# Optimization experiments

Hardware: AMD Instinct MI355X
Metric: run time of the kernel (lower is better)

Reference implementation:

```python
import jax, jax.numpy as jnp
import numpy as np

B, T, C, H = 2, 2048, 1024, 16
DH = C // H  # 64


def setup_inputs() -> dict:
    key = jax.random.key(0)
    ks = jax.random.split(key, 8)
    scale = 1.0 / np.sqrt(C)
    x = jax.random.normal(ks[0], (B, T, C), dtype=jnp.float32)
    mask = jax.random.randint(ks[1], (B, T), 0, 2, dtype=jnp.int32)
    Wq = jax.random.normal(ks[2], (C, C), dtype=jnp.float32) * scale
    bq = jnp.zeros((C,), dtype=jnp.float32)
    Wk = jax.random.normal(ks[3], (C, C), dtype=jnp.float32) * scale
    bk = jnp.zeros((C,), dtype=jnp.float32)
    Wv = jax.random.normal(ks[4], (C, C), dtype=jnp.float32) * scale
    bv = jnp.zeros((C,), dtype=jnp.float32)
    return {"x": x, "Wq": Wq, "bq": bq, "Wk": Wk, "bk": bk, "Wv": Wv, "bv": bv, "mask": mask}


def reference(x, Wq, bq, Wk, bk, Wv, bv, mask):
    # q/k/v projections: [B,T,C] -> [B,H,T,DH]
    def proj(W, b):
        return (x @ W + b).reshape(B, T, H, DH).transpose(0, 2, 1, 3)

    q = proj(Wq, bq)
    k = proj(Wk, bk)
    v = proj(Wv, bv)

    att = jnp.einsum("bhqd,bhkd->bhqk", q, k) * (1.0 / np.sqrt(DH))

    # outer-product padding mask: square_mask[b,q,k] = mask[b,q]*mask[b,k]
    m = mask.astype(jnp.float32)
    square_mask = m[:, :, None] * m[:, None, :]           # [B,T,T]
    sm = (square_mask != 0)[:, None, :, :]                 # [B,1,T,T]
    att = jnp.where(sm, att, -jnp.inf)

    # rows that are fully masked (query token padded) -> softmax gives NaN
    # in torch; torch then zeros the NaNs. Replicate with a safe softmax.
    row_valid = (mask != 0)[:, None, :, None]              # [B,1,T,1]
    att_safe = jnp.where(row_valid, att, 0.0)
    att = jax.nn.softmax(att_safe, axis=-1)
    att = jnp.where(row_valid, att, 0.0)
    # attn_pdrop = 0.0 -> dropout is identity

    y = jnp.einsum("bhqk,bhkd->bhqd", att, v)              # [B,H,T,DH]
    y = y.transpose(0, 2, 1, 3).reshape(B, T, C)
    return y
```

## Files before the change

### kernel.cpp

```cpp
#include <hip/hip_runtime.h>

#define B_ 2
#define T_ 2048
#define C_ 1024
#define H_ 16
#define DH_ 64

typedef __attribute__((ext_vector_type(8))) _Float16 half8;
typedef __attribute__((ext_vector_type(2))) __fp16 fp16x2;
typedef __attribute__((ext_vector_type(4))) float f32x4;

__device__ __forceinline__ unsigned short f2h(float f) {
    union { _Float16 h; unsigned short u; } cv; cv.h = (_Float16)f; return cv.u;
}
__device__ __forceinline__ unsigned pk2(float a, float b) {
    union { fp16x2 h; unsigned u; } cv;
    cv.h = __builtin_amdgcn_cvt_pkrtz(a, b);
    return cv.u;
}

__device__ __forceinline__ void gll16(const void* g, void* l) {
    __builtin_amdgcn_global_load_lds(
        (const __attribute__((address_space(1))) void*)g,
        (__attribute__((address_space(3))) void*)l, 16, 0, 0);
}

__global__ __launch_bounds__(256) void prep_x_kernel(
    const float* __restrict__ x, unsigned short* __restrict__ xf,
    const int* __restrict__ mask, unsigned short* __restrict__ mb)
{
    const size_t idx8 = ((size_t)blockIdx.x * 256 + threadIdx.x) * 8;
    float4 v0 = *(const float4*)(x + idx8);
    float4 v1 = *(const float4*)(x + idx8 + 4);
    float f[8] = {v0.x, v0.y, v0.z, v0.w, v1.x, v1.y, v1.z, v1.w};
    unsigned short h[8];
#pragma unroll
    for (int i = 0; i < 8; i++) h[i] = f2h(f[i]);
    *(uint4*)(xf + idx8) = *(const uint4*)h;

    if (blockIdx.x == 0) {
#pragma unroll
        for (int j = 0; j < 16; j++) {
            int i = threadIdx.x * 16 + j;
            mb[i] = (mask[i] != 0) ? (unsigned short)0x3C00 : (unsigned short)0;
        }
    }
}

__global__ __launch_bounds__(256) void prep_w_kernel(
    const float* __restrict__ Wq, const float* __restrict__ Wk,
    const float* __restrict__ Wv, unsigned short* __restrict__ wt)
{
    __shared__ float tile[32][33];
    const int z = blockIdx.z;
    const float* __restrict__ W = (z == 0) ? Wq : (z == 1) ? Wk : Wv;
    unsigned short* __restrict__ wtz = wt + (size_t)z * C_ * C_;
    const int n0 = blockIdx.x * 32;
    const int k0 = blockIdx.y * 32;
    const int tx = threadIdx.x;
    const int ty = threadIdx.y;
#pragma unroll
    for (int j = 0; j < 4; j++)
        tile[ty + j * 8][tx] = W[(size_t)(k0 + ty + j * 8) * C_ + n0 + tx];
    __syncthreads();
#pragma unroll
    for (int j = 0; j < 4; j++)
        wtz[(size_t)(n0 + ty + j * 8) * C_ + k0 + tx] = f2h(tile[tx][ty + j * 8]);
}

__global__ __launch_bounds__(256) void qkv_mfma_kernel(
    const unsigned short* __restrict__ xf, const unsigned short* __restrict__ wt,
    const float* __restrict__ bq, const float* __restrict__ bk,
    const float* __restrict__ bv, const int* __restrict__ maskp,
    unsigned short* __restrict__ qb, unsigned short* __restrict__ kb,
    unsigned short* __restrict__ vt)
{
    __shared__ unsigned short sX[128 * 64];
    __shared__ unsigned short sW[128 * 64];

    const int z = blockIdx.z;
    const float* __restrict__ bias = (z == 0) ? bq : (z == 1) ? bk : bv;
    const unsigned short* __restrict__ wtz = wt + (size_t)z * C_ * C_;

    const int tok0 = blockIdx.x * 128;
    const int col0 = blockIdx.y * 128;
    const int wv    = threadIdx.x >> 6;
    const int lane  = threadIdx.x & 63;
    const int l15   = lane & 15;
    const int quad  = lane >> 4;
    const int l7    = l15 & 7;
    const int wm    = wv >> 1;
    const int wn    = wv & 1;
    const int lrow8 = lane >> 3;
    const int gch   = (lane & 7) ^ lrow8;

    f32x4 acc[4][4];
#pragma unroll
    for (int i = 0; i < 4; i++)
#pragma unroll
        for (int j = 0; j < 4; j++) acc[i][j] = (f32x4){0.f, 0.f, 0.f, 0.f};

    int aoff[4][2], boff[4][2];
#pragma unroll
    for (int i = 0; i < 4; i++)
#pragma unroll
        for (int s = 0; s < 2; s++) {
            aoff[i][s] = (wm * 64 + i * 16 + l15) * 64 + (((s * 4 + quad) ^ l7) * 8);
            boff[i][s] = (wn * 64 + i * 16 + l15) * 64 + (((s * 4 + quad) ^ l7) * 8);
        }

    const unsigned short* Abuf = (z < 2) ? sX : sW;
    const unsigned short* Bbuf = (z < 2) ? sW : sX;

    for (int k0 = 0; k0 < C_; k0 += 64) {
        __syncthreads();
#pragma unroll
        for (int s = 0; s < 8; ++s) {
            int g    = (s << 2) + wv;
            int tsel = g >> 4;
            int r0   = (g & 15) << 3;
            const unsigned short* src = tsel ? wtz : xf;
            unsigned short*       dst = tsel ? sW  : sX;
            int rowg = tsel ? col0 : tok0;
            gll16(src + (size_t)(rowg + r0 + lrow8) * C_ + k0 + gch * 8,
                  dst + r0 * 64);
        }
        __syncthreads();

        half8 af[4][2], bf_[4][2];
#pragma unroll
        for (int i = 0; i < 4; i++)
#pragma unroll
            for (int s = 0; s < 2; s++) {
                af[i][s]  = *(const half8*)&Abuf[aoff[i][s]];
                bf_[i][s] = *(const half8*)&Bbuf[boff[i][s]];
            }
#pragma unroll
        for (int s = 0; s < 2; s++)
#pragma unroll
            for (int j = 0; j < 4; j++)
#pragma unroll
                for (int i = 0; i < 4; i++)
                    acc[i][j] = __builtin_amdgcn_mfma_f32_16x16x32_f16(
                        af[i][s], bf_[j][s], acc[i][j], 0, 0, 0);
    }

    if (z < 2) {
        unsigned short* outp = (z == 0) ? qb : kb;
#pragma unroll
        for (int j = 0; j < 4; j++) {
            int col = col0 + wn * 64 + j * 16 + l15;
            int h = col >> 6, d = col & 63;
            float bs = bias[col];
#pragma unroll
            for (int i = 0; i < 4; i++) {
#pragma unroll
                for (int r = 0; r < 4; r++) {
                    int tok = tok0 + wm * 64 + i * 16 + quad * 4 + r;
                    int bidx = tok >> 11, t = tok & (T_ - 1);
                    outp[((size_t)(bidx * H_ + h) * T_ + t) * DH_ + d] =
                        f2h(acc[i][j][r] + bs);
                }
            }
        }
    } else {
        float mv4[4]; int bidx4[4], t4[4];
#pragma unroll
        for (int j = 0; j < 4; j++) {
            int tok = tok0 + wn * 64 + j * 16 + l15;
            bidx4[j] = tok >> 11; t4[j] = tok & (T_ - 1);
            mv4[j] = (maskp[bidx4[j] * T_ + t4[j]] != 0) ? 1.f : 0.f;
        }
#pragma unroll
        for (int i = 0; i < 4; i++) {
#pragma unroll
            for (int r = 0; r < 4; r++) {
                int col = col0 + wm * 64 + i * 16 + quad * 4 + r;
                int h = col >> 6, d = col & 63;
                float bs = bias[col];
#pragma unroll
                for (int j = 0; j < 4; j++) {
                    vt[((size_t)(bidx4[j] * H_ + h) * DH_ + d) * T_ + t4[j]] =
                        f2h((acc[i][j][r] + bs) * mv4[j]);
                }
            }
        }
    }
}

__global__ __launch_bounds__(256) void attn_mfma_kernel(
    const unsigned short* __restrict__ qb,
    const unsigned short* __restrict__ kb,
    const unsigned short* __restrict__ vt,
    const int* __restrict__ mask,
    const unsigned short* __restrict__ mb,
    float* __restrict__ out)
{
    __shared__ unsigned short Ks[2][64 * 64];
    __shared__ unsigned short Vs[2][64 * 64];
    __shared__ unsigned short Ps[4][16 * 64];

    const int bh   = blockIdx.x;
    const int b    = bh >> 4;
    const int h    = bh & 15;
    const int wv   = threadIdx.x >> 6;
    const int lane = threadIdx.x & 63;
    const int l15  = lane & 15;
    const int quad = lane >> 4;
    const int l7   = l15 & 7;
    const int q0w  = blockIdx.y * 128 + wv * 32;

    const unsigned short* kbh = kb + (size_t)bh * T_ * DH_;
    const unsigned short* vbh = vt + (size_t)bh * DH_ * T_;
    const unsigned short* mbb = mb + b * T_;
    const int* __restrict__ mrow = mask + b * T_;

    half8 qf[2][2];
#pragma unroll
    for (int qt = 0; qt < 2; ++qt)
#pragma unroll
        for (int c = 0; c < 2; ++c)
            qf[qt][c] = *(const half8*)(qb + ((size_t)bh * T_ + q0w + qt * 16 + l15) * DH_
                                        + c * 32 + quad * 8);

    f32x4 o[2][4];
#pragma unroll
    for (int qt = 0; qt < 2; ++qt)
#pragma unroll
        for (int n = 0; n < 4; ++n) o[qt][n] = (f32x4){0.f, 0.f, 0.f, 0.f};
    f32x4 lacc[2];
    lacc[0] = (f32x4){0.f, 0.f, 0.f, 0.f};
    lacc[1] = (f32x4){0.f, 0.f, 0.f, 0.f};

    const int lrow = lane >> 3;
    const int gch  = (lane & 7) ^ lrow;

#pragma unroll
    for (int s = 0; s < 4; ++s) {
        int j  = (wv << 2) + s;
        int rb = j & 7;
        if (j < 8) gll16(kbh + (size_t)(rb * 8 + lrow) * DH_ + gch * 8, &Ks[0][rb * 512]);
        else       gll16(vbh + (size_t)(rb * 8 + lrow) * T_  + gch * 8, &Vs[0][rb * 512]);
    }

    for (int kt = 0; kt < 32; ++kt) {
        const int cur   = kt & 1;
        const int kbase = kt * 64;
        __syncthreads();

        if (kt < 31) {
            const int nb = kbase + 64;
#pragma unroll
            for (int s = 0; s < 4; ++s) {
                int j  = (wv << 2) + s;
                int rb = j & 7;
                if (j < 8) gll16(kbh + (size_t)(nb + rb * 8 + lrow) * DH_ + gch * 8,
                                 &Ks[cur ^ 1][rb * 512]);
                else       gll16(vbh + (size_t)(rb * 8 + lrow) * T_ + nb + gch * 8,
                                 &Vs[cur ^ 1][rb * 512]);
            }
        }

        const unsigned short* Kc = &Ks[cur][0];
        const unsigned short* Vc = &Vs[cur][0];

        half8 kf[4][2], vf[4][2];
#pragma unroll
        for (int ktile = 0; ktile < 4; ++ktile)
#pragma unroll
            for (int c = 0; c < 2; ++c) {
                kf[ktile][c] = *(const half8*)(Kc + (ktile * 16 + l15) * 64
                                               + (((c * 4 + quad) ^ l7) * 8));
                vf[ktile][c] = *(const half8*)(Vc + (ktile * 16 + l15) * 64
                                               + (((c * 4 + quad) ^ l7) * 8));
            }

        half8 bmf[2];
#pragma unroll
        for (int kc = 0; kc < 2; ++kc) {
            half8 mv = *(const half8*)(mbb + kbase + kc * 32 + quad * 8);
            bmf[kc] = (l15 == 0) ? mv : (half8)0;
        }

#pragma unroll
        for (int qt = 0; qt < 2; ++qt) {
            unsigned short* Pq = &Ps[wv][0];

#pragma unroll
            for (int ktile = 0; ktile < 4; ++ktile) {
                f32x4 st = (f32x4){0.f, 0.f, 0.f, 0.f};
                st = __builtin_amdgcn_mfma_f32_16x16x32_f16(kf[ktile][0], qf[qt][0], st, 0, 0, 0);
                st = __builtin_amdgcn_mfma_f32_16x16x32_f16(kf[ktile][1], qf[qt][1], st, 0, 0, 0);
                float p0 = __builtin_amdgcn_exp2f(fminf(st[0] * 0.18033688011112042f, 14.f));
                float p1 = __builtin_amdgcn_exp2f(fminf(st[1] * 0.18033688011112042f, 14.f));
                float p2 = __builtin_amdgcn_exp2f(fminf(st[2] * 0.18033688011112042f, 14.f));
                float p3 = __builtin_amdgcn_exp2f(fminf(st[3] * 0.18033688011112042f, 14.f));
                uint2 pk;
                pk.x = pk2(p0, p1);
                pk.y = pk2(p2, p3);
                *(uint2*)(Pq + l15 * 64 + (((ktile * 2 + (quad >> 1)) ^ l7) * 8)
                          + (quad & 1) * 4) = pk;
            }

            half8 pf[2];
#pragma unroll
            for (int kc = 0; kc < 2; ++kc)
                pf[kc] = *(const half8*)(Pq + l15 * 64 + (((kc * 4 + quad) ^ l7) * 8));

            lacc[qt] = __builtin_amdgcn_mfma_f32_16x16x32_f16(pf[0], bmf[0], lacc[qt], 0, 0, 0);
            lacc[qt] = __builtin_amdgcn_mfma_f32_16x16x32_f16(pf[1], bmf[1], lacc[qt], 0, 0, 0);

#pragma unroll
            for (int n = 0; n < 4; ++n) {
#pragma unroll
                for (int kc = 0; kc < 2; ++kc)
                    o[qt][n] = __builtin_amdgcn_mfma_f32_16x16x32_f16(
                        pf[kc], vf[n][kc], o[qt][n], 0, 0, 0);
            }
        }
    }

#pragma unroll
    for (int qt = 0; qt < 2; ++qt) {
#pragma unroll
        for (int r = 0; r < 4; ++r) {
            float lv = __shfl(lacc[qt][r], quad << 4, 64);
            int q = q0w + qt * 16 + quad * 4 + r;
            float iv = (mrow[q] != 0 && lv > 0.f) ? (1.0f / lv) : 0.f;
            float* orow = out + ((size_t)(b * T_ + q)) * C_ + h * DH_;
#pragma unroll
            for (int n = 0; n < 4; ++n)
                orow[n * 16 + l15] = o[qt][n][r] * iv;
        }
    }
}

extern "C" void kernel_launch(void* const* d_in, const int* in_sizes, int n_in,
                              void* d_out, int out_size, void* d_ws, size_t ws_size,
                              hipStream_t stream)
{
    (void)in_sizes; (void)n_in; (void)out_size; (void)ws_size;
    const float* x  = (const float*)d_in[0];
    const float* Wq = (const float*)d_in[1];
    const float* bq = (const float*)d_in[2];
    const float* Wk = (const float*)d_in[3];
    const float* bk = (const float*)d_in[4];
    const float* Wv = (const float*)d_in[5];
    const float* bv = (const float*)d_in[6];
    const int* mask = (const int*)d_in[7];
    float* out = (float*)d_out;

    const size_t NX = (size_t)B_ * T_ * C_;
    unsigned short* xf = (unsigned short*)d_ws;
    unsigned short* wt = xf + NX;
    unsigned short* qb = wt + (size_t)3 * C_ * C_;
    unsigned short* kb = qb + NX;
    unsigned short* vt = kb + NX;
    unsigned short* mb = vt + NX;

    prep_x_kernel<<<2048, 256, 0, stream>>>(x, xf, mask, mb);
    prep_w_kernel<<<dim3(32, 32, 3), dim3(32, 8), 0, stream>>>(Wq, Wk, Wv, wt);
    qkv_mfma_kernel<<<dim3(32, 8, 3), 256, 0, stream>>>(
        xf, wt, bq, bk, bv, mask, qb, kb, vt);
    attn_mfma_kernel<<<dim3(32, 16), 256, 0, stream>>>(qb, kb, vt, mask, mb, out);
}
```

Measured before the change: 177.7 us.

## Split attention key range across two blocks and add a combine kernel

Adds a second grid dimension so each attention block handles half of the key sequence (1024 keys), doubling the number of blocks to raise GPU occupancy. Each half writes unnormalized partial outputs and per-row softmax denominators; a new combine kernel sums the two partials, applies the mask, and normalizes. This works because the kernel accumulates exp sums without a running max, so partials add linearly. The cost is an extra kernel launch plus writing and re-reading a full fp32 partial output. That partial buffer reuses the workspace left by the x/W conversion buffers and may extend past them.

```diff
diff --git a/kernel.cpp b/kernel.cpp
--- a/kernel.cpp
+++ b/kernel.cpp
@@ -192,9 +192,10 @@
     const unsigned short* __restrict__ qb,
     const unsigned short* __restrict__ kb,
     const unsigned short* __restrict__ vt,
-    const int* __restrict__ mask,
     const unsigned short* __restrict__ mb,
-    float* __restrict__ out)
+    float* __restrict__ po0,
+    float* __restrict__ po1,
+    float* __restrict__ lw)
 {
     __shared__ unsigned short Ks[2][64 * 64];
     __shared__ unsigned short Vs[2][64 * 64];
@@ -203,6 +204,8 @@
     const int bh   = blockIdx.x;
     const int b    = bh >> 4;
     const int h    = bh & 15;
+    const int kh   = blockIdx.z;
+    const int kh0  = kh << 10;
     const int wv   = threadIdx.x >> 6;
     const int lane = threadIdx.x & 63;
     const int l15  = lane & 15;
@@ -210,10 +213,12 @@
     const int l7   = l15 & 7;
     const int q0w  = blockIdx.y * 128 + wv * 32;
 
+    float* __restrict__ po = kh ? po1 : po0;
+    float* __restrict__ lwk = lw + (size_t)kh * B_ * T_ * H_;
+
     const unsigned short* kbh = kb + (size_t)bh * T_ * DH_;
     const unsigned short* vbh = vt + (size_t)bh * DH_ * T_;
     const unsigned short* mbb = mb + b * T_;
-    const int* __restrict__ mrow = mask + b * T_;
 
     half8 qf[2][2];
 #pragma unroll
@@ -239,16 +244,16 @@
     for (int s = 0; s < 4; ++s) {
         int j  = (wv << 2) + s;
         int rb = j & 7;
-        if (j < 8) gll16(kbh + (size_t)(rb * 8 + lrow) * DH_ + gch * 8, &Ks[0][rb * 512]);
-        else       gll16(vbh + (size_t)(rb * 8 + lrow) * T_  + gch * 8, &Vs[0][rb * 512]);
-    }
-
-    for (int kt = 0; kt < 32; ++kt) {
+        if (j < 8) gll16(kbh + (size_t)(kh0 + rb * 8 + lrow) * DH_ + gch * 8, &Ks[0][rb * 512]);
+        else       gll16(vbh + (size_t)(rb * 8 + lrow) * T_ + kh0 + gch * 8, &Vs[0][rb * 512]);
+    }
+
+    for (int kt = 0; kt < 16; ++kt) {
         const int cur   = kt & 1;
-        const int kbase = kt * 64;
+        const int kbase = kh0 + kt * 64;
         __syncthreads();
 
-        if (kt < 31) {
+        if (kt < 15) {
             const int nb = kbase + 64;
 #pragma unroll
             for (int s = 0; s < 4; ++s) {
@@ -324,15 +329,40 @@
     for (int qt = 0; qt < 2; ++qt) {
 #pragma unroll
         for (int r = 0; r < 4; ++r) {
-            float lv = __shfl(lacc[qt][r], quad << 4, 64);
             int q = q0w + qt * 16 + quad * 4 + r;
-            float iv = (mrow[q] != 0 && lv > 0.f) ? (1.0f / lv) : 0.f;
-            float* orow = out + ((size_t)(b * T_ + q)) * C_ + h * DH_;
+            float* orow = po + ((size_t)(b * T_ + q)) * C_ + h * DH_;
 #pragma unroll
             for (int n = 0; n < 4; ++n)
-                orow[n * 16 + l15] = o[qt][n][r] * iv;
-        }
-    }
+                orow[n * 16 + l15] = o[qt][n][r];
+            if (l15 == 0)
+                lwk[((size_t)(b * T_ + q)) * H_ + h] = lacc[qt][r];
+        }
+    }
+}
+
+__global__ __launch_bounds__(256) void combine_kernel(
+    const float* __restrict__ po1, const float* __restrict__ lw,
+    const int* __restrict__ mask, float* __restrict__ out)
+{
+    const size_t e = ((size_t)blockIdx.x * 256 + threadIdx.x) * 8;
+    const int h = (int)((e >> 6) & 15);
+    const int q = (int)((e >> 10) & (T_ - 1));
+    const int b = (int)(e >> 21);
+
+    float4 a0 = *(const float4*)(out + e);
+    float4 a1 = *(const float4*)(out + e + 4);
+    float4 c0 = *(const float4*)(po1 + e);
+    float4 c1 = *(const float4*)(po1 + e + 4);
+    size_t li = ((size_t)(b * T_ + q)) * H_ + h;
+    float l = lw[li] + lw[(size_t)B_ * T_ * H_ + li];
+    float iv = (mask[b * T_ + q] != 0 && l > 0.f) ? (1.0f / l) : 0.f;
+
+    float4 r0 = {(a0.x + c0.x) * iv, (a0.y + c0.y) * iv,
+                 (a0.z + c0.z) * iv, (a0.w + c0.w) * iv};
+    float4 r1 = {(a1.x + c1.x) * iv, (a1.y + c1.y) * iv,
+                 (a1.z + c1.z) * iv, (a1.w + c1.w) * iv};
+    *(float4*)(out + e)     = r0;
+    *(float4*)(out + e + 4) = r1;
 }
 
 extern "C" void kernel_launch(void* const* d_in, const int* in_sizes, int n_in,
@@ -351,16 +381,20 @@
     float* out = (float*)d_out;
 
     const size_t NX = (size_t)B_ * T_ * C_;
-    unsigned short* xf = (unsigned short*)d_ws;
-    unsigned short* wt = xf + NX;
-    unsigned short* qb = wt + (size_t)3 * C_ * C_;
+    unsigned short* qb = (unsigned short*)d_ws;
     unsigned short* kb = qb + NX;
     unsigned short* vt = kb + NX;
     unsigned short* mb = vt + NX;
+    unsigned short* xf = mb + (size_t)B_ * T_;
+    unsigned short* wt = xf + NX;
+    float* po1 = (float*)xf;
+    float* lw  = po1 + NX;
 
     prep_x_kernel<<<2048, 256, 0, stream>>>(x, xf, mask, mb);
     prep_w_kernel<<<dim3(32, 32, 3), dim3(32, 8), 0, stream>>>(Wq, Wk, Wv, wt);
     qkv_mfma_kernel<<<dim3(32, 8, 3), 256, 0, stream>>>(
         xf, wt, bq, bk, bv, mask, qb, kb, vt);
-    attn_mfma_kernel<<<dim3(32, 16), 256, 0, stream>>>(qb, kb, vt, mask, mb, out);
-}
+    attn_mfma_kernel<<<dim3(32, 16, 2), 256, 0, stream>>>(
+        qb, kb, vt, mb, out, po1, lw);
+    combine_kernel<<<2048, 256, 0, stream>>>(po1, lw, mask, out);
+}
```

Measured after the change: 189.6 us. 6.7% more time.

## Store K/V in MFMA fragment order and load directly to registers

Applied to the files above, without the earlier changes.

The QKV projection now writes K and V into a pre-swizzled fragment-major layout that matches the per-lane MFMA operand order. This lets the attention kernel read each fragment with contiguous 16-byte global loads instead of staging K/V tiles through double-buffered LDS with global_load_lds and a per-iteration barrier. The per-wave P buffer is also split per query tile, which avoids reuse hazards without sync. In exchange, every wave fetches K/V from global memory or L2 on its own with no sharing across the block, and there is no explicit prefetch to hide load latency.

```diff
diff --git a/kernel.cpp b/kernel.cpp
--- a/kernel.cpp
+++ b/kernel.cpp
@@ -23,6 +23,15 @@
     __builtin_amdgcn_global_load_lds(
         (const __attribute__((address_space(1))) void*)g,
         (__attribute__((address_space(3))) void*)l, 16, 0, 0);
+}
+
+__device__ __forceinline__ size_t kidx(int bh, int key, int d) {
+    return ((size_t)(bh * 128 + (key >> 4)) * 2 + (d >> 5)) * 512
+         + (size_t)((((d >> 3) & 3) * 16 + (key & 15)) * 8 + (d & 7));
+}
+__device__ __forceinline__ size_t vidx(int bh, int key, int d) {
+    return (((size_t)(bh * 32 + (key >> 6)) * 4 + (d >> 4)) * 2 + ((key >> 5) & 1)) * 512
+         + (size_t)((((key >> 3) & 3) * 16 + (d & 15)) * 8 + (key & 7));
 }
 
 __global__ __launch_bounds__(256) void prep_x_kernel(
@@ -72,8 +81,8 @@
     const unsigned short* __restrict__ xf, const unsigned short* __restrict__ wt,
     const float* __restrict__ bq, const float* __restrict__ bk,
     const float* __restrict__ bv, const int* __restrict__ maskp,
-    unsigned short* __restrict__ qb, unsigned short* __restrict__ kb,
-    unsigned short* __restrict__ vt)
+    unsigned short* __restrict__ qb, unsigned short* __restrict__ kfr,
+    unsigned short* __restrict__ vfr)
 {
     __shared__ unsigned short sX[128 * 64];
     __shared__ unsigned short sW[128 * 64];
@@ -145,8 +154,7 @@
                         af[i][s], bf_[j][s], acc[i][j], 0, 0, 0);
     }
 
-    if (z < 2) {
-        unsigned short* outp = (z == 0) ? qb : kb;
+    if (z == 0) {
 #pragma unroll
         for (int j = 0; j < 4; j++) {
             int col = col0 + wn * 64 + j * 16 + l15;
@@ -158,8 +166,24 @@
                 for (int r = 0; r < 4; r++) {
                     int tok = tok0 + wm * 64 + i * 16 + quad * 4 + r;
                     int bidx = tok >> 11, t = tok & (T_ - 1);
-                    outp[((size_t)(bidx * H_ + h) * T_ + t) * DH_ + d] =
+                    qb[((size_t)(bidx * H_ + h) * T_ + t) * DH_ + d] =
                         f2h(acc[i][j][r] + bs);
+                }
+            }
+        }
+    } else if (z == 1) {
+#pragma unroll
+        for (int j = 0; j < 4; j++) {
+            int col = col0 + wn * 64 + j * 16 + l15;
+            int h = col >> 6, d = col & 63;
+            float bs = bias[col];
+#pragma unroll
+            for (int i = 0; i < 4; i++) {
+#pragma unroll
+                for (int r = 0; r < 4; r++) {
+                    int tok = tok0 + wm * 64 + i * 16 + quad * 4 + r;
+                    int bidx = tok >> 11, t = tok & (T_ - 1);
+                    kfr[kidx(bidx * H_ + h, t, d)] = f2h(acc[i][j][r] + bs);
                 }
             }
         }
@@ -180,7 +204,7 @@
                 float bs = bias[col];
 #pragma unroll
                 for (int j = 0; j < 4; j++) {
-                    vt[((size_t)(bidx4[j] * H_ + h) * DH_ + d) * T_ + t4[j]] =
+                    vfr[vidx(bidx4[j] * H_ + h, t4[j], d)] =
                         f2h((acc[i][j][r] + bs) * mv4[j]);
                 }
             }
@@ -190,15 +214,13 @@
 
 __global__ __launch_bounds__(256) void attn_mfma_kernel(
     const unsigned short* __restrict__ qb,
-    const unsigned short* __restrict__ kb,
-    const unsigned short* __restrict__ vt,
+    const unsigned short* __restrict__ kfr,
+    const unsigned short* __restrict__ vfr,
     const int* __restrict__ mask,
     const unsigned short* __restrict__ mb,
     float* __restrict__ out)
 {
-    __shared__ unsigned short Ks[2][64 * 64];
-    __shared__ unsigned short Vs[2][64 * 64];
-    __shared__ unsigned short Ps[4][16 * 64];
+    __shared__ unsigned short Ps[4][2][16 * 64];
 
     const int bh   = blockIdx.x;
     const int b    = bh >> 4;
@@ -210,10 +232,11 @@
     const int l7   = l15 & 7;
     const int q0w  = blockIdx.y * 128 + wv * 32;
 
-    const unsigned short* kbh = kb + (size_t)bh * T_ * DH_;
-    const unsigned short* vbh = vt + (size_t)bh * DH_ * T_;
     const unsigned short* mbb = mb + b * T_;
     const int* __restrict__ mrow = mask + b * T_;
+
+    const unsigned short* kfp = kfr + (size_t)bh * 131072 + lane * 8;
+    const unsigned short* vfp = vfr + (size_t)bh * 131072 + lane * 8;
 
     half8 qf[2][2];
 #pragma unroll
@@ -232,48 +255,17 @@
     lacc[0] = (f32x4){0.f, 0.f, 0.f, 0.f};
     lacc[1] = (f32x4){0.f, 0.f, 0.f, 0.f};
 
-    const int lrow = lane >> 3;
-    const int gch  = (lane & 7) ^ lrow;
-
-#pragma unroll
-    for (int s = 0; s < 4; ++s) {
-        int j  = (wv << 2) + s;
-        int rb = j & 7;
-        if (j < 8) gll16(kbh + (size_t)(rb * 8 + lrow) * DH_ + gch * 8, &Ks[0][rb * 512]);
-        else       gll16(vbh + (size_t)(rb * 8 + lrow) * T_  + gch * 8, &Vs[0][rb * 512]);
-    }
-
     for (int kt = 0; kt < 32; ++kt) {
-        const int cur   = kt & 1;
         const int kbase = kt * 64;
-        __syncthreads();
-
-        if (kt < 31) {
-            const int nb = kbase + 64;
-#pragma unroll
-            for (int s = 0; s < 4; ++s) {
-                int j  = (wv << 2) + s;
-                int rb = j & 7;
-                if (j < 8) gll16(kbh + (size_t)(nb + rb * 8 + lrow) * DH_ + gch * 8,
-                                 &Ks[cur ^ 1][rb * 512]);
-                else       gll16(vbh + (size_t)(rb * 8 + lrow) * T_ + nb + gch * 8,
-                                 &Vs[cur ^ 1][rb * 512]);
-            }
-        }
-
-        const unsigned short* Kc = &Ks[cur][0];
-        const unsigned short* Vc = &Vs[cur][0];
 
         half8 kf[4][2], vf[4][2];
 #pragma unroll
-        for (int ktile = 0; ktile < 4; ++ktile)
-#pragma unroll
-            for (int c = 0; c < 2; ++c) {
-                kf[ktile][c] = *(const half8*)(Kc + (ktile * 16 + l15) * 64
-                                               + (((c * 4 + quad) ^ l7) * 8));
-                vf[ktile][c] = *(const half8*)(Vc + (ktile * 16 + l15) * 64
-                                               + (((c * 4 + quad) ^ l7) * 8));
-            }
+        for (int s = 0; s < 8; ++s)
+            kf[s >> 1][s & 1] = *(const half8*)(kfp + s * 512);
+#pragma unroll
+        for (int s = 0; s < 8; ++s)
+            vf[s >> 1][s & 1] = *(const half8*)(vfp + s * 512);
+        kfp += 4096; vfp += 4096;
 
         half8 bmf[2];
 #pragma unroll
@@ -284,7 +276,7 @@
 
 #pragma unroll
         for (int qt = 0; qt < 2; ++qt) {
-            unsigned short* Pq = &Ps[wv][0];
+            unsigned short* Pq = &Ps[wv][qt][0];
 
 #pragma unroll
             for (int ktile = 0; ktile < 4; ++ktile) {
@@ -351,16 +343,16 @@
     float* out = (float*)d_out;
 
     const size_t NX = (size_t)B_ * T_ * C_;
-    unsigned short* xf = (unsigned short*)d_ws;
-    unsigned short* wt = xf + NX;
-    unsigned short* qb = wt + (size_t)3 * C_ * C_;
-    unsigned short* kb = qb + NX;
-    unsigned short* vt = kb + NX;
-    unsigned short* mb = vt + NX;
+    unsigned short* xf  = (unsigned short*)d_ws;
+    unsigned short* wt  = xf + NX;
+    unsigned short* qb  = wt + (size_t)3 * C_ * C_;
+    unsigned short* kfr = qb + NX;
+    unsigned short* vfr = kfr + NX;
+    unsigned short* mb  = vfr + NX;
 
     prep_x_kernel<<<2048, 256, 0, stream>>>(x, xf, mask, mb);
     prep_w_kernel<<<dim3(32, 32, 3), dim3(32, 8), 0, stream>>>(Wq, Wk, Wv, wt);
     qkv_mfma_kernel<<<dim3(32, 8, 3), 256, 0, stream>>>(
-        xf, wt, bq, bk, bv, mask, qb, kb, vt);
-    attn_mfma_kernel<<<dim3(32, 16), 256, 0, stream>>>(qb, kb, vt, mask, mb, out);
-}
+        xf, wt, bq, bk, bv, mask, qb, kfr, vfr);
+    attn_mfma_kernel<<<dim3(32, 16), 256, 0, stream>>>(qb, kfr, vfr, mask, mb, out);
+}
```

Result: slower. 189.5 us (+6.7%).
